# Performance work log

Measured on AMD Instinct MI355X. Metric: run time of the kernel, lower is better.

The kernel has to match this reference:

```python
import jax, jax.numpy as jnp
import numpy as np

N = 6144
HIDDEN = 48
HEADS = 3
HEAD = HIDDEN // HEADS


def setup_inputs() -> dict:
    key = jax.random.key(0)
    ks = jax.random.split(key, 8)
    s = 1.0 / np.sqrt(HIDDEN)
    A = (jax.random.uniform(ks[0], (N, N)) < 0.05).astype(jnp.float32)
    h = jax.random.normal(ks[1], (N, HIDDEN), dtype=jnp.float32)
    Wq = jax.random.normal(ks[2], (HIDDEN, HIDDEN), dtype=jnp.float32) * s
    Wk = jax.random.normal(ks[3], (HIDDEN, HIDDEN), dtype=jnp.float32) * s
    Wv = jax.random.normal(ks[4], (HIDDEN, HIDDEN), dtype=jnp.float32) * s
    bq = jnp.zeros((HIDDEN,), jnp.float32)
    bk = jnp.zeros((HIDDEN,), jnp.float32)
    bv = jnp.zeros((HIDDEN,), jnp.float32)
    return {"A": A, "h": h, "Wq": Wq, "bq": bq, "Wk": Wk, "bk": bk, "Wv": Wv, "bv": bv}


def reference(A, h, Wq, bq, Wk, bk, Wv, bv):
    n = h.shape[0]
    # QKV projections (torch Linear: x @ W.T + b)
    q = (h @ Wq.T + bq).reshape(n, HEADS, HEAD).transpose(1, 0, 2)  # [H,N,d]
    k = (h @ Wk.T + bk).reshape(n, HEADS, HEAD).transpose(1, 0, 2)
    v = (h @ Wv.T + bv).reshape(n, HEADS, HEAD).transpose(1, 0, 2)
    # scores = (q k^T) * A / N**(-0.5)  == (q k^T) * A * sqrt(N)  (faithful to source)
    scale = jnp.asarray(n, h.dtype) ** 0.5
    scores = jnp.einsum("hnd,hmd->hnm", q, k) * A[None, :, :] * scale
    scores = jax.nn.softmax(scores, axis=2)
    out = jnp.einsum("hnm,hmd->hnd", scores, v)  # [H,N,d]
    out = out.transpose(1, 0, 2).reshape(n, HIDDEN)
    return (out, scores)
```

## Files before the change

### kernel.cpp

```cpp
#include <hip/hip_runtime.h>
#include <math.h>

#define NN   6144
#define HID  48
#define BLK  256
#define RPB  2
#define CAP  448
#define CTOT (RPB*CAP)
#define SCALE 78.38367176906175f
#define NBLK (NN/RPB)

typedef float vf4 __attribute__((ext_vector_type(4)));

__global__ __launch_bounds__(256)
void qkv_kernel(const float* __restrict__ h,
                const float* __restrict__ Wq, const float* __restrict__ bq,
                const float* __restrict__ Wk, const float* __restrict__ bk,
                const float* __restrict__ Wv, const float* __restrict__ bv,
                float* __restrict__ qw, float* __restrict__ kw, float* __restrict__ vw) {
    int idx = blockIdx.x * blockDim.x + threadIdx.x;
    int i = idx / HID, c = idx % HID;
    const float4* h4  = (const float4*)(h + (size_t)i * HID);
    const float4* wq4 = (const float4*)(Wq + (size_t)c * HID);
    const float4* wk4 = (const float4*)(Wk + (size_t)c * HID);
    const float4* wv4 = (const float4*)(Wv + (size_t)c * HID);
    float aq = 0.f, ak = 0.f, av = 0.f;
    #pragma unroll
    for (int r = 0; r < HID / 4; ++r) {
        float4 hv = h4[r];
        float4 q4 = wq4[r], k4 = wk4[r], v4 = wv4[r];
        aq = fmaf(hv.x, q4.x, aq); aq = fmaf(hv.y, q4.y, aq);
        aq = fmaf(hv.z, q4.z, aq); aq = fmaf(hv.w, q4.w, aq);
        ak = fmaf(hv.x, k4.x, ak); ak = fmaf(hv.y, k4.y, ak);
        ak = fmaf(hv.z, k4.z, ak); ak = fmaf(hv.w, k4.w, ak);
        av = fmaf(hv.x, v4.x, av); av = fmaf(hv.y, v4.y, av);
        av = fmaf(hv.w, v4.w, av); av = fmaf(hv.z, v4.z, av);
    }
    aq += bq[c]; ak += bk[c]; av += bv[c];
    int head = c >> 4, d = c & 15;
    size_t off = ((size_t)head * NN + i) * 16 + d;
    qw[off] = aq; kw[off] = ak; vw[off] = av;
}

__global__ __launch_bounds__(256)
void vtot_kernel(const float* __restrict__ vw, float* __restrict__ vtot) {
    int c = blockIdx.x;
    int head = c >> 4, d = c & 15;
    float s = 0.f;
    for (int j = threadIdx.x; j < NN; j += 256)
        s += vw[((size_t)head * NN + j) * 16 + d];
    #pragma unroll
    for (int o = 32; o; o >>= 1) s += __shfl_xor(s, o, 64);
    __shared__ float red[4];
    int wid = threadIdx.x >> 6, lane = threadIdx.x & 63;
    if (lane == 0) red[wid] = s;
    __syncthreads();
    if (threadIdx.x == 0) vtot[c] = red[0] + red[1] + red[2] + red[3];
}

__global__ __launch_bounds__(BLK, 8)
void attn_kernel(const float* __restrict__ A,
                 const float* __restrict__ qw, const float* __restrict__ kw,
                 const float* __restrict__ vw, const float* __restrict__ vtot,
                 float* __restrict__ out) {
    __shared__ int   list[CTOT];
    __shared__ float sc[3][CTOT];
    __shared__ __align__(16) float qs[RPB * 48];
    __shared__ float wredML[4 * 6 * 2];
    __shared__ float MF[6], ZF[6], IVF[6];
    __shared__ unsigned wsc[4];

    const int i0 = blockIdx.x * RPB;
    const int tid = threadIdx.x;
    const int wid = tid >> 6, lane = tid & 63;

    if (tid < RPB * 48) {
        int r = tid / 48, c = tid % 48;
        int hh = c >> 4, d = c & 15;
        qs[tid] = qw[((size_t)hh * NN + (i0 + r)) * 16 + d];
    }

    unsigned mr[RPB];
    #pragma unroll
    for (int r = 0; r < RPB; ++r) {
        const vf4* Ar = (const vf4*)(A + (size_t)(i0 + r) * NN);
        unsigned mm = 0u;
        #pragma unroll
        for (int c = 0; c < 6; ++c) {
            vf4 a4 = __builtin_nontemporal_load(&Ar[tid + c * BLK]);
            int p = c * 4;
            if (a4.x != 0.f) mm |= 1u << (p + 0);
            if (a4.y != 0.f) mm |= 1u << (p + 1);
            if (a4.z != 0.f) mm |= 1u << (p + 2);
            if (a4.w != 0.f) mm |= 1u << (p + 3);
        }
        mr[r] = mm;
    }
    unsigned lo = (unsigned)__popc(mr[0]) | ((unsigned)__popc(mr[1]) << 16);

    unsigned il = lo;
    #pragma unroll
    for (int o = 1; o < 64; o <<= 1) {
        unsigned pl = __shfl_up(il, o, 64);
        if (lane >= o) il += pl;
    }
    if (lane == 63) wsc[wid] = il;
    __syncthreads();
    unsigned bl = il - lo, tl = 0;
    #pragma unroll
    for (int w = 0; w < 4; ++w) {
        unsigned a = wsc[w];
        if (w < wid) bl += a;
        tl += a;
    }
    const int C0 = min((int)(tl & 0xFFFFu), CAP), C1 = min((int)(tl >> 16), CAP);
    int Cr2[2] = {C0, C1};
    int cu[3] = {0, C0, C0 + C1};
    int bs[2] = {(int)(bl & 0xFFFFu), (int)(bl >> 16)};

    #pragma unroll
    for (int r = 0; r < RPB; ++r) {
        unsigned m = mr[r];
        int b = bs[r];
        while (m) {
            int p = __ffs(m) - 1; m &= m - 1;
            if (b < CAP) list[cu[r] + b] = 4 * (tid + (p >> 2) * BLK) + (p & 3);
            ++b;
        }
    }
    __syncthreads();

    {
        const int q4 = tid >> 2, part = tid & 3;
        #pragma unroll
        for (int r = 0; r < RPB; ++r) {
            float4 qv0 = ((const float4*)(qs + r * 48 +  0))[part];
            float4 qv1 = ((const float4*)(qs + r * 48 + 16))[part];
            float4 qv2 = ((const float4*)(qs + r * 48 + 32))[part];
            float mA = 0.f, lA = 0.f, mB = 0.f, lB = 0.f, mC = 0.f, lC = 0.f;
            for (int e = cu[r] + q4; e < cu[r + 1]; e += (BLK >> 2)) {
                int j = list[e];
                float4 k0 = ((const float4*)(kw + ((size_t)0 * NN + j) * 16))[part];
                float4 k1 = ((const float4*)(kw + ((size_t)1 * NN + j) * 16))[part];
                float4 k2 = ((const float4*)(kw + ((size_t)2 * NN + j) * 16))[part];
                float d0 = k0.x * qv0.x; d0 = fmaf(k0.y, qv0.y, d0);
                d0 = fmaf(k0.z, qv0.z, d0); d0 = fmaf(k0.w, qv0.w, d0);
                float d1 = k1.x * qv1.x; d1 = fmaf(k1.y, qv1.y, d1);
                d1 = fmaf(k1.z, qv1.z, d1); d1 = fmaf(k1.w, qv1.w, d1);
                float d2 = k2.x * qv2.x; d2 = fmaf(k2.y, qv2.y, d2);
                d2 = fmaf(k2.z, qv2.z, d2); d2 = fmaf(k2.w, qv2.w, d2);
                d0 += __shfl_xor(d0, 1, 64); d0 += __shfl_xor(d0, 2, 64);
                d1 += __shfl_xor(d1, 1, 64); d1 += __shfl_xor(d1, 2, 64);
                d2 += __shfl_xor(d2, 1, 64); d2 += __shfl_xor(d2, 2, 64);
                float s0 = d0 * SCALE, s1 = d1 * SCALE, s2 = d2 * SCALE;
                if (part == 0) sc[0][e] = s0;
                else if (part == 1) sc[1][e] = s1;
                else if (part == 2) sc[2][e] = s2;
                float nm;
                nm = fmaxf(mA, s0); lA = lA * __expf(mA - nm) + __expf(s0 - nm); mA = nm;
                nm = fmaxf(mB, s1); lB = lB * __expf(mB - nm) + __expf(s1 - nm); mB = nm;
                nm = fmaxf(mC, s2); lC = lC * __expf(mC - nm) + __expf(s2 - nm); mC = nm;
            }
            #pragma unroll
            for (int o = 4; o < 64; o <<= 1) {
                float om, ol, nm;
                om = __shfl_xor(mA, o, 64); ol = __shfl_xor(lA, o, 64);
                nm = fmaxf(mA, om); lA = lA * __expf(mA - nm) + ol * __expf(om - nm); mA = nm;
                om = __shfl_xor(mB, o, 64); ol = __shfl_xor(lB, o, 64);
                nm = fmaxf(mB, om); lB = lB * __expf(mB - nm) + ol * __expf(om - nm); mB = nm;
                om = __shfl_xor(mC, o, 64); ol = __shfl_xor(lC, o, 64);
                nm = fmaxf(mC, om); lC = lC * __expf(mC - nm) + ol * __expf(om - nm); mC = nm;
            }
            if (lane == 0) {
                int b0 = (wid * 6 + r * 3) * 2;
                wredML[b0 + 0] = mA; wredML[b0 + 1] = lA;
                wredML[b0 + 2] = mB; wredML[b0 + 3] = lB;
                wredML[b0 + 4] = mC; wredML[b0 + 5] = lC;
            }
        }
    }
    __syncthreads();

    if (tid < 6) {
        int r = tid / 3;
        float M = wredML[tid * 2], L = wredML[tid * 2 + 1];
        #pragma unroll
        for (int w = 1; w < 4; ++w) {
            float mw = wredML[(w * 6 + tid) * 2], lw = wredML[(w * 6 + tid) * 2 + 1];
            float nm = fmaxf(M, mw);
            L = L * __expf(M - nm) + lw * __expf(mw - nm);
            M = nm;
        }
        float z = __expf(-M);
        MF[tid] = M; ZF[tid] = z;
        IVF[tid] = 1.0f / (L + (float)(NN - Cr2[r]) * z);
    }
    __syncthreads();

    if (wid < 3) {
        const int h = wid, rr4 = lane & 3, a = lane >> 2;
        const float* vbase = vw + (size_t)h * NN * 16 + rr4 * 4;
        #pragma unroll
        for (int r = 0; r < RPB; ++r) {
            int s = r * 3 + h;
            float M = MF[s], zz = ZF[s], iv = IVF[s];
            float ax = 0.f, ay = 0.f, az = 0.f, aw = 0.f;
            #pragma unroll 2
            for (int e = cu[r] + a; e < cu[r + 1]; e += 16) {
                float p = __expf(sc[h][e] - M);
                float w = p - zz;
                int j = list[e];
                float4 vv = *(const float4*)(vbase + (size_t)j * 16);
                ax = fmaf(w, vv.x, ax); ay = fmaf(w, vv.y, ay);
                az = fmaf(w, vv.z, az); aw = fmaf(w, vv.w, aw);
            }
            #pragma unroll
            for (int o = 4; o < 64; o <<= 1) {
                ax += __shfl_xor(ax, o, 64); ay += __shfl_xor(ay, o, 64);
                az += __shfl_xor(az, o, 64); aw += __shfl_xor(aw, o, 64);
            }
            if (a == 0) {
                int c0 = h * 16 + rr4 * 4;
                float4 vt = *(const float4*)(vtot + c0);
                float4 o4;
                o4.x = (ax + zz * vt.x) * iv;
                o4.y = (ay + zz * vt.y) * iv;
                o4.z = (az + zz * vt.z) * iv;
                o4.w = (aw + zz * vt.w) * iv;
                *(float4*)(out + (size_t)(i0 + r) * HID + c0) = o4;
            }
        }
    }

    float* Pp = out + (size_t)NN * HID;
    const size_t NSQ = (size_t)NN * NN;
    #pragma unroll
    for (int r = 0; r < RPB; ++r) {
        int s = r * 3;
        float M0 = MF[s], M1 = MF[s + 1], M2 = MF[s + 2];
        float iv0 = IVF[s], iv1 = IVF[s + 1], iv2 = IVF[s + 2];
        float zi0 = ZF[s] * iv0, zi1 = ZF[s + 1] * iv1, zi2 = ZF[s + 2] * iv2;
        size_t rowoff = (size_t)(i0 + r) * NN;
        unsigned msk = mr[r];
        #pragma unroll
        for (int c = 0; c < 6; ++c) {
            unsigned nib = (msk >> (c * 4)) & 0xFu;
            int idx = bs[r] + __popc(msk & ((1u << (c * 4)) - 1u));
            vf4 P0, P1, P2;
            #pragma unroll
            for (int e = 0; e < 4; ++e) {
                int nz = (int)((nib >> e) & 1u);
                if (nz && idx < CAP) {
                    int slot = cu[r] + idx;
                    P0[e] = __expf(sc[0][slot] - M0) * iv0;
                    P1[e] = __expf(sc[1][slot] - M1) * iv1;
                    P2[e] = __expf(sc[2][slot] - M2) * iv2;
                } else { P0[e] = zi0; P1[e] = zi1; P2[e] = zi2; }
                idx += nz;
            }
            __builtin_nontemporal_store(P0, &((vf4*)(Pp + rowoff))[tid + c * BLK]);
            __builtin_nontemporal_store(P1, &((vf4*)(Pp + NSQ + rowoff))[tid + c * BLK]);
            __builtin_nontemporal_store(P2, &((vf4*)(Pp + 2 * NSQ + rowoff))[tid + c * BLK]);
        }
    }
}

extern "C" void kernel_launch(void* const* d_in, const int* in_sizes, int n_in,
                              void* d_out, int out_size, void* d_ws, size_t ws_size,
                              hipStream_t stream) {
    const float* A  = (const float*)d_in[0];
    const float* h  = (const float*)d_in[1];
    const float* Wq = (const float*)d_in[2];
    const float* bq = (const float*)d_in[3];
    const float* Wk = (const float*)d_in[4];
    const float* bk = (const float*)d_in[5];
    const float* Wv = (const float*)d_in[6];
    const float* bv = (const float*)d_in[7];
    float* out = (float*)d_out;
    float* ws  = (float*)d_ws;

    float* qw   = ws;
    float* kw   = ws + (size_t)3 * NN * 16;
    float* vw   = ws + (size_t)6 * NN * 16;
    float* vtot = ws + (size_t)9 * NN * 16;

    qkv_kernel<<<(NN * HID) / 256, 256, 0, stream>>>(h, Wq, bq, Wk, bk, Wv, bv, qw, kw, vw);
    vtot_kernel<<<HID, 256, 0, stream>>>(vw, vtot);
    attn_kernel<<<NBLK, BLK, 0, stream>>>(A, qw, kw, vw, vtot, out);
}
```

Baseline: 627.2 us.

## Assign one wavefront per row and drop block-wide syncs and index lists

The attention kernel now gives each 64-lane wavefront its own row instead of splitting two rows across a 256-thread block. Each lane walks its own nonzero bitmask directly, computing full 16-wide dot products and V accumulations per neighbour. This removes the shared index list, the cross-wave scan and all __syncthreads, and keeps the softmax reductions inside the wave. The cost is more register pressure (48 accumulators plus q values), load imbalance between lanes with different nonzero counts, and uncoalesced per-lane gathers of K/V rows.

```diff
diff --git a/kernel.cpp b/kernel.cpp
--- a/kernel.cpp
+++ b/kernel.cpp
@@ -3,14 +3,42 @@
 
 #define NN   6144
 #define HID  48
-#define BLK  256
-#define RPB  2
 #define CAP  448
-#define CTOT (RPB*CAP)
 #define SCALE 78.38367176906175f
-#define NBLK (NN/RPB)
+#define HS   ((size_t)NN * 16)
 
 typedef float vf4 __attribute__((ext_vector_type(4)));
+
+#define DOT16(s, qa, qb, qc, qd, kp) do {                                   \
+    vf4 A_ = (kp)[0], B_ = (kp)[1], C_ = (kp)[2], D_ = (kp)[3];             \
+    s = qa.x * A_.x; s = fmaf(qa.y, A_.y, s);                               \
+    s = fmaf(qa.z, A_.z, s); s = fmaf(qa.w, A_.w, s);                       \
+    s = fmaf(qb.x, B_.x, s); s = fmaf(qb.y, B_.y, s);                       \
+    s = fmaf(qb.z, B_.z, s); s = fmaf(qb.w, B_.w, s);                       \
+    s = fmaf(qc.x, C_.x, s); s = fmaf(qc.y, C_.y, s);                       \
+    s = fmaf(qc.z, C_.z, s); s = fmaf(qc.w, C_.w, s);                       \
+    s = fmaf(qd.x, D_.x, s); s = fmaf(qd.y, D_.y, s);                       \
+    s = fmaf(qd.z, D_.z, s); s = fmaf(qd.w, D_.w, s); } while (0)
+
+#define VACC4(acc, W_, kv) {                                                \
+    acc.x = fmaf(W_, kv.x, acc.x); acc.y = fmaf(W_, kv.y, acc.y);           \
+    acc.z = fmaf(W_, kv.z, acc.z); acc.w = fmaf(W_, kv.w, acc.w); }
+
+#define RED4(v) {                                                           \
+    v.x += __shfl_xor(v.x, o, 64); v.y += __shfl_xor(v.y, o, 64);           \
+    v.z += __shfl_xor(v.z, o, 64); v.w += __shfl_xor(v.w, o, 64); }
+
+#define MLMERGE(m, l) {                                                     \
+    float om_ = __shfl_xor(m, o, 64), ol_ = __shfl_xor(l, o, 64);           \
+    float nm_ = fmaxf(m, om_);                                              \
+    l = l * __expf(m - nm_) + ol_ * __expf(om_ - nm_); m = nm_; }
+
+#define OUTW(acc, hh, ti, zz, iv) {                                         \
+    vf4 vt4 = ((const vf4*)vtot)[(hh) * 4 + (ti)];                          \
+    vf4 o4;                                                                 \
+    o4.x = (acc.x + zz * vt4.x) * iv; o4.y = (acc.y + zz * vt4.y) * iv;     \
+    o4.z = (acc.z + zz * vt4.z) * iv; o4.w = (acc.w + zz * vt4.w) * iv;     \
+    ((vf4*)(out + (size_t)row * HID))[(hh) * 4 + (ti)] = o4; }
 
 __global__ __launch_bounds__(256)
 void qkv_kernel(const float* __restrict__ h,
@@ -58,209 +86,166 @@
     if (threadIdx.x == 0) vtot[c] = red[0] + red[1] + red[2] + red[3];
 }
 
-__global__ __launch_bounds__(BLK, 8)
+__global__ __launch_bounds__(256)
 void attn_kernel(const float* __restrict__ A,
                  const float* __restrict__ qw, const float* __restrict__ kw,
                  const float* __restrict__ vw, const float* __restrict__ vtot,
                  float* __restrict__ out) {
-    __shared__ int   list[CTOT];
-    __shared__ float sc[3][CTOT];
-    __shared__ __align__(16) float qs[RPB * 48];
-    __shared__ float wredML[4 * 6 * 2];
-    __shared__ float MF[6], ZF[6], IVF[6];
-    __shared__ unsigned wsc[4];
-
-    const int i0 = blockIdx.x * RPB;
+    __shared__ float sc[4][3][CAP];
     const int tid = threadIdx.x;
     const int wid = tid >> 6, lane = tid & 63;
-
-    if (tid < RPB * 48) {
-        int r = tid / 48, c = tid % 48;
-        int hh = c >> 4, d = c & 15;
-        qs[tid] = qw[((size_t)hh * NN + (i0 + r)) * 16 + d];
-    }
-
-    unsigned mr[RPB];
-    #pragma unroll
-    for (int r = 0; r < RPB; ++r) {
-        const vf4* Ar = (const vf4*)(A + (size_t)(i0 + r) * NN);
-        unsigned mm = 0u;
+    const int row = blockIdx.x * 4 + wid;
+    float* s0w = &sc[wid][0][0];
+    float* s1w = &sc[wid][1][0];
+    float* s2w = &sc[wid][2][0];
+
+    const vf4* qp0 = (const vf4*)(qw + (size_t)row * 16);
+    const vf4* qp1 = (const vf4*)(qw + HS + (size_t)row * 16);
+    const vf4* qp2 = (const vf4*)(qw + 2 * HS + (size_t)row * 16);
+    vf4 q00 = qp0[0], q01 = qp0[1], q02 = qp0[2], q03 = qp0[3];
+    vf4 q10 = qp1[0], q11 = qp1[1], q12 = qp1[2], q13 = qp1[3];
+    vf4 q20 = qp2[0], q21 = qp2[1], q22 = qp2[2], q23 = qp2[3];
+
+    unsigned m0 = 0, m1 = 0, m2 = 0;
+    const vf4* Ar = (const vf4*)(A + (size_t)row * NN);
+    #pragma unroll
+    for (int c = 0; c < 24; ++c) {
+        vf4 a4 = __builtin_nontemporal_load(&Ar[c * 64 + lane]);
+        unsigned acc = 0, bit = 1u << ((c & 7) * 4);
+        if (a4.x != 0.f) acc |= bit;
+        if (a4.y != 0.f) acc |= bit << 1;
+        if (a4.z != 0.f) acc |= bit << 2;
+        if (a4.w != 0.f) acc |= bit << 3;
+        if (c < 8) m0 |= acc; else if (c < 16) m1 |= acc; else m2 |= acc;
+    }
+
+    const int cnt = __popc(m0) + __popc(m1) + __popc(m2);
+    int incl = cnt;
+    #pragma unroll
+    for (int o = 1; o < 64; o <<= 1) {
+        int p = __shfl_up(incl, o, 64);
+        if (lane >= o) incl += p;
+    }
+    const int base = incl - cnt;
+    const int C = min(__shfl(incl, 63, 64), CAP);
+
+    float mA = 0.f, lA = 0.f, mB = 0.f, lB = 0.f, mC = 0.f, lC = 0.f;
+    {
+        unsigned mw[3] = {m0, m1, m2};
+        int b = base;
         #pragma unroll
-        for (int c = 0; c < 6; ++c) {
-            vf4 a4 = __builtin_nontemporal_load(&Ar[tid + c * BLK]);
-            int p = c * 4;
-            if (a4.x != 0.f) mm |= 1u << (p + 0);
-            if (a4.y != 0.f) mm |= 1u << (p + 1);
-            if (a4.z != 0.f) mm |= 1u << (p + 2);
-            if (a4.w != 0.f) mm |= 1u << (p + 3);
-        }
-        mr[r] = mm;
-    }
-    unsigned lo = (unsigned)__popc(mr[0]) | ((unsigned)__popc(mr[1]) << 16);
-
-    unsigned il = lo;
-    #pragma unroll
-    for (int o = 1; o < 64; o <<= 1) {
-        unsigned pl = __shfl_up(il, o, 64);
-        if (lane >= o) il += pl;
-    }
-    if (lane == 63) wsc[wid] = il;
-    __syncthreads();
-    unsigned bl = il - lo, tl = 0;
-    #pragma unroll
-    for (int w = 0; w < 4; ++w) {
-        unsigned a = wsc[w];
-        if (w < wid) bl += a;
-        tl += a;
-    }
-    const int C0 = min((int)(tl & 0xFFFFu), CAP), C1 = min((int)(tl >> 16), CAP);
-    int Cr2[2] = {C0, C1};
-    int cu[3] = {0, C0, C0 + C1};
-    int bs[2] = {(int)(bl & 0xFFFFu), (int)(bl >> 16)};
-
-    #pragma unroll
-    for (int r = 0; r < RPB; ++r) {
-        unsigned m = mr[r];
-        int b = bs[r];
-        while (m) {
-            int p = __ffs(m) - 1; m &= m - 1;
-            if (b < CAP) list[cu[r] + b] = 4 * (tid + (p >> 2) * BLK) + (p & 3);
-            ++b;
-        }
-    }
-    __syncthreads();
-
-    {
-        const int q4 = tid >> 2, part = tid & 3;
-        #pragma unroll
-        for (int r = 0; r < RPB; ++r) {
-            float4 qv0 = ((const float4*)(qs + r * 48 +  0))[part];
-            float4 qv1 = ((const float4*)(qs + r * 48 + 16))[part];
-            float4 qv2 = ((const float4*)(qs + r * 48 + 32))[part];
-            float mA = 0.f, lA = 0.f, mB = 0.f, lB = 0.f, mC = 0.f, lC = 0.f;
-            for (int e = cu[r] + q4; e < cu[r + 1]; e += (BLK >> 2)) {
-                int j = list[e];
-                float4 k0 = ((const float4*)(kw + ((size_t)0 * NN + j) * 16))[part];
-                float4 k1 = ((const float4*)(kw + ((size_t)1 * NN + j) * 16))[part];
-                float4 k2 = ((const float4*)(kw + ((size_t)2 * NN + j) * 16))[part];
-                float d0 = k0.x * qv0.x; d0 = fmaf(k0.y, qv0.y, d0);
-                d0 = fmaf(k0.z, qv0.z, d0); d0 = fmaf(k0.w, qv0.w, d0);
-                float d1 = k1.x * qv1.x; d1 = fmaf(k1.y, qv1.y, d1);
-                d1 = fmaf(k1.z, qv1.z, d1); d1 = fmaf(k1.w, qv1.w, d1);
-                float d2 = k2.x * qv2.x; d2 = fmaf(k2.y, qv2.y, d2);
-                d2 = fmaf(k2.z, qv2.z, d2); d2 = fmaf(k2.w, qv2.w, d2);
-                d0 += __shfl_xor(d0, 1, 64); d0 += __shfl_xor(d0, 2, 64);
-                d1 += __shfl_xor(d1, 1, 64); d1 += __shfl_xor(d1, 2, 64);
-                d2 += __shfl_xor(d2, 1, 64); d2 += __shfl_xor(d2, 2, 64);
-                float s0 = d0 * SCALE, s1 = d1 * SCALE, s2 = d2 * SCALE;
-                if (part == 0) sc[0][e] = s0;
-                else if (part == 1) sc[1][e] = s1;
-                else if (part == 2) sc[2][e] = s2;
-                float nm;
-                nm = fmaxf(mA, s0); lA = lA * __expf(mA - nm) + __expf(s0 - nm); mA = nm;
-                nm = fmaxf(mB, s1); lB = lB * __expf(mB - nm) + __expf(s1 - nm); mB = nm;
-                nm = fmaxf(mC, s2); lC = lC * __expf(mC - nm) + __expf(s2 - nm); mC = nm;
-            }
-            #pragma unroll
-            for (int o = 4; o < 64; o <<= 1) {
-                float om, ol, nm;
-                om = __shfl_xor(mA, o, 64); ol = __shfl_xor(lA, o, 64);
-                nm = fmaxf(mA, om); lA = lA * __expf(mA - nm) + ol * __expf(om - nm); mA = nm;
-                om = __shfl_xor(mB, o, 64); ol = __shfl_xor(lB, o, 64);
-                nm = fmaxf(mB, om); lB = lB * __expf(mB - nm) + ol * __expf(om - nm); mB = nm;
-                om = __shfl_xor(mC, o, 64); ol = __shfl_xor(lC, o, 64);
-                nm = fmaxf(mC, om); lC = lC * __expf(mC - nm) + ol * __expf(om - nm); mC = nm;
-            }
-            if (lane == 0) {
-                int b0 = (wid * 6 + r * 3) * 2;
-                wredML[b0 + 0] = mA; wredML[b0 + 1] = lA;
-                wredML[b0 + 2] = mB; wredML[b0 + 3] = lB;
-                wredML[b0 + 4] = mC; wredML[b0 + 5] = lC;
+        for (int w = 0; w < 3; ++w) {
+            unsigned mm = mw[w];
+            while (mm) {
+                int p = __ffs(mm) - 1; mm &= mm - 1;
+                int j = (w * 8 + (p >> 2)) * 256 + lane * 4 + (p & 3);
+                if (b < CAP) {
+                    const vf4* kp0 = (const vf4*)(kw + (size_t)j * 16);
+                    const vf4* kp1 = (const vf4*)(kw + HS + (size_t)j * 16);
+                    const vf4* kp2 = (const vf4*)(kw + 2 * HS + (size_t)j * 16);
+                    float s0, s1, s2;
+                    DOT16(s0, q00, q01, q02, q03, kp0);
+                    DOT16(s1, q10, q11, q12, q13, kp1);
+                    DOT16(s2, q20, q21, q22, q23, kp2);
+                    s0 *= SCALE; s1 *= SCALE; s2 *= SCALE;
+                    s0w[b] = s0; s1w[b] = s1; s2w[b] = s2;
+                    float nm;
+                    nm = fmaxf(mA, s0); lA = lA * __expf(mA - nm) + __expf(s0 - nm); mA = nm;
+                    nm = fmaxf(mB, s1); lB = lB * __expf(mB - nm) + __expf(s1 - nm); mB = nm;
+                    nm = fmaxf(mC, s2); lC = lC * __expf(mC - nm) + __expf(s2 - nm); mC = nm;
+                }
+                ++b;
             }
         }
     }
-    __syncthreads();
-
-    if (tid < 6) {
-        int r = tid / 3;
-        float M = wredML[tid * 2], L = wredML[tid * 2 + 1];
+
+    #pragma unroll
+    for (int o = 1; o < 64; o <<= 1) {
+        MLMERGE(mA, lA); MLMERGE(mB, lB); MLMERGE(mC, lC);
+    }
+    const float M0 = mA, M1 = mB, M2 = mC;
+    const float z0 = __expf(-M0), z1 = __expf(-M1), z2 = __expf(-M2);
+    const float fc = (float)(NN - C);
+    const float iv0 = 1.0f / (lA + fc * z0);
+    const float iv1 = 1.0f / (lB + fc * z1);
+    const float iv2 = 1.0f / (lC + fc * z2);
+
+    vf4 zero = {0.f, 0.f, 0.f, 0.f};
+    vf4 a00 = zero, a01 = zero, a02 = zero, a03 = zero;
+    vf4 a10 = zero, a11 = zero, a12 = zero, a13 = zero;
+    vf4 a20 = zero, a21 = zero, a22 = zero, a23 = zero;
+    {
+        unsigned mw[3] = {m0, m1, m2};
+        int b = base;
         #pragma unroll
-        for (int w = 1; w < 4; ++w) {
-            float mw = wredML[(w * 6 + tid) * 2], lw = wredML[(w * 6 + tid) * 2 + 1];
-            float nm = fmaxf(M, mw);
-            L = L * __expf(M - nm) + lw * __expf(mw - nm);
-            M = nm;
-        }
-        float z = __expf(-M);
-        MF[tid] = M; ZF[tid] = z;
-        IVF[tid] = 1.0f / (L + (float)(NN - Cr2[r]) * z);
-    }
-    __syncthreads();
-
-    if (wid < 3) {
-        const int h = wid, rr4 = lane & 3, a = lane >> 2;
-        const float* vbase = vw + (size_t)h * NN * 16 + rr4 * 4;
-        #pragma unroll
-        for (int r = 0; r < RPB; ++r) {
-            int s = r * 3 + h;
-            float M = MF[s], zz = ZF[s], iv = IVF[s];
-            float ax = 0.f, ay = 0.f, az = 0.f, aw = 0.f;
-            #pragma unroll 2
-            for (int e = cu[r] + a; e < cu[r + 1]; e += 16) {
-                float p = __expf(sc[h][e] - M);
-                float w = p - zz;
-                int j = list[e];
-                float4 vv = *(const float4*)(vbase + (size_t)j * 16);
-                ax = fmaf(w, vv.x, ax); ay = fmaf(w, vv.y, ay);
-                az = fmaf(w, vv.z, az); aw = fmaf(w, vv.w, aw);
-            }
-            #pragma unroll
-            for (int o = 4; o < 64; o <<= 1) {
-                ax += __shfl_xor(ax, o, 64); ay += __shfl_xor(ay, o, 64);
-                az += __shfl_xor(az, o, 64); aw += __shfl_xor(aw, o, 64);
-            }
-            if (a == 0) {
-                int c0 = h * 16 + rr4 * 4;
-                float4 vt = *(const float4*)(vtot + c0);
-                float4 o4;
-                o4.x = (ax + zz * vt.x) * iv;
-                o4.y = (ay + zz * vt.y) * iv;
-                o4.z = (az + zz * vt.z) * iv;
-                o4.w = (aw + zz * vt.w) * iv;
-                *(float4*)(out + (size_t)(i0 + r) * HID + c0) = o4;
+        for (int w = 0; w < 3; ++w) {
+            unsigned mm = mw[w];
+            while (mm) {
+                int p = __ffs(mm) - 1; mm &= mm - 1;
+                int j = (w * 8 + (p >> 2)) * 256 + lane * 4 + (p & 3);
+                if (b < CAP) {
+                    float w0 = __expf(s0w[b] - M0) - z0;
+                    float w1 = __expf(s1w[b] - M1) - z1;
+                    float w2 = __expf(s2w[b] - M2) - z2;
+                    const vf4* vp0 = (const vf4*)(vw + (size_t)j * 16);
+                    const vf4* vp1 = (const vf4*)(vw + HS + (size_t)j * 16);
+                    const vf4* vp2 = (const vf4*)(vw + 2 * HS + (size_t)j * 16);
+                    vf4 t;
+                    t = vp0[0]; VACC4(a00, w0, t); t = vp0[1]; VACC4(a01, w0, t);
+                    t = vp0[2]; VACC4(a02, w0, t); t = vp0[3]; VACC4(a03, w0, t);
+                    t = vp1[0]; VACC4(a10, w1, t); t = vp1[1]; VACC4(a11, w1, t);
+                    t = vp1[2]; VACC4(a12, w1, t); t = vp1[3]; VACC4(a13, w1, t);
+                    t = vp2[0]; VACC4(a20, w2, t); t = vp2[1]; VACC4(a21, w2, t);
+                    t = vp2[2]; VACC4(a22, w2, t); t = vp2[3]; VACC4(a23, w2, t);
+                }
+                ++b;
             }
         }
     }
+    #pragma unroll
+    for (int o = 32; o; o >>= 1) {
+        RED4(a00); RED4(a01); RED4(a02); RED4(a03);
+        RED4(a10); RED4(a11); RED4(a12); RED4(a13);
+        RED4(a20); RED4(a21); RED4(a22); RED4(a23);
+    }
+    if (lane == 0) {
+        OUTW(a00, 0, 0, z0, iv0); OUTW(a01, 0, 1, z0, iv0);
+        OUTW(a02, 0, 2, z0, iv0); OUTW(a03, 0, 3, z0, iv0);
+        OUTW(a10, 1, 0, z1, iv1); OUTW(a11, 1, 1, z1, iv1);
+        OUTW(a12, 1, 2, z1, iv1); OUTW(a13, 1, 3, z1, iv1);
+        OUTW(a20, 2, 0, z2, iv2); OUTW(a21, 2, 1, z2, iv2);
+        OUTW(a22, 2, 2, z2, iv2); OUTW(a23, 2, 3, z2, iv2);
+    }
 
     float* Pp = out + (size_t)NN * HID;
     const size_t NSQ = (size_t)NN * NN;
-    #pragma unroll
-    for (int r = 0; r < RPB; ++r) {
-        int s = r * 3;
-        float M0 = MF[s], M1 = MF[s + 1], M2 = MF[s + 2];
-        float iv0 = IVF[s], iv1 = IVF[s + 1], iv2 = IVF[s + 2];
-        float zi0 = ZF[s] * iv0, zi1 = ZF[s + 1] * iv1, zi2 = ZF[s + 2] * iv2;
-        size_t rowoff = (size_t)(i0 + r) * NN;
-        unsigned msk = mr[r];
+    const float zi0 = z0 * iv0, zi1 = z1 * iv1, zi2 = z2 * iv2;
+    size_t rowoff = (size_t)row * NN;
+    {
+        unsigned mw[3] = {m0, m1, m2};
+        int b = base;
         #pragma unroll
-        for (int c = 0; c < 6; ++c) {
-            unsigned nib = (msk >> (c * 4)) & 0xFu;
-            int idx = bs[r] + __popc(msk & ((1u << (c * 4)) - 1u));
-            vf4 P0, P1, P2;
+        for (int w = 0; w < 3; ++w) {
+            unsigned mm = mw[w];
             #pragma unroll
-            for (int e = 0; e < 4; ++e) {
-                int nz = (int)((nib >> e) & 1u);
-                if (nz && idx < CAP) {
-                    int slot = cu[r] + idx;
-                    P0[e] = __expf(sc[0][slot] - M0) * iv0;
-                    P1[e] = __expf(sc[1][slot] - M1) * iv1;
-                    P2[e] = __expf(sc[2][slot] - M2) * iv2;
-                } else { P0[e] = zi0; P1[e] = zi1; P2[e] = zi2; }
-                idx += nz;
+            for (int cc = 0; cc < 8; ++cc) {
+                unsigned nib = (mm >> (cc * 4)) & 0xFu;
+                vf4 P0, P1, P2;
+                #pragma unroll
+                for (int e = 0; e < 4; ++e) {
+                    int nz = (int)((nib >> e) & 1u);
+                    if (nz && b < CAP) {
+                        P0[e] = __expf(s0w[b] - M0) * iv0;
+                        P1[e] = __expf(s1w[b] - M1) * iv1;
+                        P2[e] = __expf(s2w[b] - M2) * iv2;
+                    } else { P0[e] = zi0; P1[e] = zi1; P2[e] = zi2; }
+                    b += nz;
+                }
+                int pi = (w * 8 + cc) * 64 + lane;
+                __builtin_nontemporal_store(P0, &((vf4*)(Pp + rowoff))[pi]);
+                __builtin_nontemporal_store(P1, &((vf4*)(Pp + NSQ + rowoff))[pi]);
+                __builtin_nontemporal_store(P2, &((vf4*)(Pp + 2 * NSQ + rowoff))[pi]);
             }
-            __builtin_nontemporal_store(P0, &((vf4*)(Pp + rowoff))[tid + c * BLK]);
-            __builtin_nontemporal_store(P1, &((vf4*)(Pp + NSQ + rowoff))[tid + c * BLK]);
-            __builtin_nontemporal_store(P2, &((vf4*)(Pp + 2 * NSQ + rowoff))[tid + c * BLK]);
         }
     }
 }
@@ -286,5 +271,5 @@
 
     qkv_kernel<<<(NN * HID) / 256, 256, 0, stream>>>(h, Wq, bq, Wk, bk, Wv, bv, qw, kw, vw);
     vtot_kernel<<<HID, 256, 0, stream>>>(vw, vtot);
-    attn_kernel<<<NBLK, BLK, 0, stream>>>(A, qw, kw, vw, vtot, out);
-}
+    attn_kernel<<<NN / 4, 256, 0, stream>>>(A, qw, kw, vw, vtot, out);
+}
```

New measurement: 652.6 us. 1.04x slower.
